# Optimization experiments

Measured on AMD Instinct MI355X. Metric: run time of the kernel, lower is better.

The kernel has to match this reference:

```python
import jax, jax.numpy as jnp
import numpy as np

TOP_K = 2

def setup_inputs() -> dict:
    key = jax.random.key(0)
    kx, kg, k1, k2 = jax.random.split(key, 4)
    B, T, D, E, H = 4, 1024, 1024, 8, 2048
    x = jax.random.normal(kx, (B, T, D), dtype=jnp.float32)
    Wg = jax.random.normal(kg, (D, E), dtype=jnp.float32) * 0.02
    W1 = jax.random.normal(k1, (E, D, H), dtype=jnp.float32) * 0.02  # c_fc per expert
    W2 = jax.random.normal(k2, (E, H, D), dtype=jnp.float32) * 0.02  # c_proj per expert
    return {"x": x, "Wg": Wg, "W1": W1, "W2": W2}

def reference(x, Wg, W1, W2):
    B, T, D = x.shape
    E = W1.shape[0]
    # Router: softmax over experts, top-k, renormalize top-k weights
    logits = jnp.einsum('btd,de->bte', x, Wg)          # (B,T,E)
    probs = jax.nn.softmax(logits, axis=-1)
    top_w, top_i = jax.lax.top_k(probs, TOP_K)          # (B,T,K)
    top_w = top_w / (jnp.sum(top_w, axis=-1, keepdims=True) + 1e-8)
    # Combine weights per (token, expert): sum_k top_w[k] * one_hot(top_i[k])
    N = B * T
    oh = jax.nn.one_hot(top_i.reshape(N, TOP_K), E, dtype=x.dtype)   # (N,K,E)
    combine = jnp.sum(oh * top_w.reshape(N, TOP_K)[..., None], axis=1)  # (N,E)
    # Expert MLPs: relu(x W1)^2 W2, evaluated densely and combined (same math)
    xt = x.reshape(N, D)
    h = jnp.einsum('td,edh->teh', xt, W1)               # (N,E,H)
    h = jnp.square(jax.nn.relu(h))
    y = jnp.einsum('teh,ehd->ted', h, W2)               # (N,E,D)
    out = jnp.einsum('te,ted->td', combine, y)          # (N,D)
    return out.reshape(B, T, D)
```

## Files before the change

kernel.cpp:

```cpp
#include <hip/hip_runtime.h>
#include <hip/hip_bf16.h>
#include <stdint.h>

#define NTOK 4096
#define DD 1024
#define EE 8
#define HH 2048
#define BM 128
#define BN 128
#define BK 64
#define MAXRB 72
#define RPAD (MAXRB*BM)
#define GG1 (8*9*(HH/BN))
#define GG2 (8*9*(DD/BN))

typedef __attribute__((ext_vector_type(4))) float f32x4;
typedef __attribute__((ext_vector_type(8))) short bf16x8;

__device__ __forceinline__ void gload16(const void* g, void* l) {
  __builtin_amdgcn_global_load_lds((const __attribute__((address_space(1))) unsigned int*)g,
                                   (__attribute__((address_space(3))) unsigned int*)l, 16, 0, 0);
}

__device__ __forceinline__ uint32_t pack_bf2(float lo, float hi) {
  return ((uint32_t)__bfloat16_as_ushort(__float2bfloat16(hi)) << 16)
       |  (uint32_t)__bfloat16_as_ushort(__float2bfloat16(lo));
}

__device__ __forceinline__ void transpose_body(uint32_t (*T)[33],
    const float* __restrict__ in, __hip_bfloat16* __restrict__ out,
    int R, int C, int tb) {
  int tilesC = C >> 6;
  int tilesPerE = (R >> 6) * tilesC;
  int e = tb / tilesPerE;
  int rem = tb % tilesPerE;
  int tr = rem / tilesC, tc = rem % tilesC;
  const float* src = in + (size_t)e * R * C + (size_t)(tr*64) * C + tc*64;
  int tid = threadIdx.x;
  int c4 = (tid & 15) << 2;
  int r2 = tid >> 4;
  #pragma unroll
  for (int i = 0; i < 2; ++i) {
    int r = r2 + (i << 4);
    const float* p0 = src + (size_t)(2*r) * C + c4;
    float4 a = *(const float4*)p0;
    float4 b = *(const float4*)(p0 + C);
    T[c4+0][r] = pack_bf2(a.x, b.x);
    T[c4+1][r] = pack_bf2(a.y, b.y);
    T[c4+2][r] = pack_bf2(a.z, b.z);
    T[c4+3][r] = pack_bf2(a.w, b.w);
  }
  __syncthreads();
  __hip_bfloat16* dst = out + (size_t)e * R * C + (size_t)(tc*64) * R + tr*64;
  int c  = tid >> 2;
  int ch = (tid & 3) * 8;
  uint32_t v[8];
  #pragma unroll
  for (int j = 0; j < 8; ++j) v[j] = T[c][ch + j];
  uint32_t* dp = (uint32_t*)(dst + (size_t)c * R + ch*2);
  #pragma unroll
  for (int j = 0; j < 8; ++j) dp[j] = v[j];
}

__global__ __launch_bounds__(256) void mega_kernel(const float* __restrict__ x,
    const float* __restrict__ Wg,
    int* __restrict__ topE, float* __restrict__ topW, int* __restrict__ counts64,
    const float* __restrict__ W1, __hip_bfloat16* __restrict__ W1bT) {
  __shared__ __align__(16) char smem[8448];
  int b = blockIdx.x;
  if (b < NTOK) {
    int t = b;
    int tid = threadIdx.x;
    const float* xr = x + (size_t)t * DD;
    double acc[EE];
    #pragma unroll
    for (int e = 0; e < EE; ++e) acc[e] = 0.0;
    #pragma unroll
    for (int i = 0; i < DD/256; ++i) {
      int d = tid + i*256;
      float xv = xr[d];
      float4 w0 = *(const float4*)(Wg + (size_t)d*EE);
      float4 w1 = *(const float4*)(Wg + (size_t)d*EE + 4);
      double xd = (double)xv;
      acc[0] += xd * (double)w0.x; acc[1] += xd * (double)w0.y;
      acc[2] += xd * (double)w0.z; acc[3] += xd * (double)w0.w;
      acc[4] += xd * (double)w1.x; acc[5] += xd * (double)w1.y;
      acc[6] += xd * (double)w1.z; acc[7] += xd * (double)w1.w;
    }
    #pragma unroll
    for (int e = 0; e < EE; ++e) {
      double v = acc[e];
      #pragma unroll
      for (int off = 32; off > 0; off >>= 1) v += __shfl_down(v, off, 64);
      acc[e] = v;
    }
    double (*sAcc)[EE] = (double(*)[EE])smem;
    int lane = tid & 63, w = tid >> 6;
    if (lane == 0) {
      #pragma unroll
      for (int e = 0; e < EE; ++e) sAcc[w][e] = acc[e];
    }
    __syncthreads();
    if (tid == 0) {
      double s[EE];
      #pragma unroll
      for (int e = 0; e < EE; ++e)
        s[e] = sAcc[0][e] + sAcc[1][e] + sAcc[2][e] + sAcc[3][e];
      double mx = s[0];
      #pragma unroll
      for (int e = 1; e < EE; ++e) mx = fmax(mx, s[e]);
      double p[EE], Z = 0.0;
      #pragma unroll
      for (int e = 0; e < EE; ++e) { p[e] = exp(s[e] - mx); Z += p[e]; }
      #pragma unroll
      for (int e = 0; e < EE; ++e) p[e] /= Z;
      int i0 = 0;
      #pragma unroll
      for (int e = 1; e < EE; ++e) if (p[e] > p[i0]) i0 = e;
      int i1 = -1;
      #pragma unroll
      for (int e = 0; e < EE; ++e) { if (e == i0) continue; if (i1 < 0 || p[e] > p[i1]) i1 = e; }
      double sm = p[i0] + p[i1] + 1e-8;
      topE[t*2]   = i0; topE[t*2+1] = i1;
      topW[t*2]   = (float)(p[i0] / sm);
      topW[t*2+1] = (float)(p[i1] / sm);
      int slot = (b & 63) * 16;
      atomicAdd(&counts64[slot + i0], 1);
      atomicAdd(&counts64[slot + i1], 1);
    }
  } else {
    transpose_body((uint32_t(*)[33])smem, W1, W1bT, DD, HH, b - NTOK);
  }
}

__global__ __launch_bounds__(1024) void assign_kernel(const int* __restrict__ counts64,
    const int* __restrict__ topE, const float* __restrict__ topW,
    int* __restrict__ po, int* __restrict__ nRB, int* __restrict__ rbExpert,
    int* __restrict__ pairsTok, float* __restrict__ pairsW, int* __restrict__ slotOf) {
  __shared__ int cnt[EE];
  __shared__ int base[EE];
  __shared__ int wcnt[16][EE];
  int tid = threadIdx.x, wv = tid >> 6, lane = tid & 63;
  if (tid < EE) {
    int s = 0;
    #pragma unroll
    for (int k = 0; k < 64; ++k) s += counts64[k*16 + tid];
    cnt[tid] = s;
  }
  for (int i = tid; i < RPAD; i += 1024) pairsTok[i] = -1;
  __syncthreads();
  if (tid == 0) {
    int off = 0;
    for (int e = 0; e < EE; ++e) {
      po[e] = off;
      off += ((cnt[e] + BM - 1) / BM) * BM;
    }
    po[EE] = off;
    *nRB = off / BM;
    int rb = 0;
    for (int e = 0; e < EE; ++e) {
      int nb = (cnt[e] + BM - 1) / BM;
      for (int b = 0; b < nb; ++b) rbExpert[rb++] = e;
    }
  }
  __syncthreads();
  if (tid < EE) base[tid] = po[tid];
  __syncthreads();
  for (int it = 0; it < 2*NTOK/1024; ++it) {
    int p = it*1024 + tid;
    int e = topE[p];
    int myrank = 0;
    #pragma unroll
    for (int ee = 0; ee < EE; ++ee) {
      unsigned long long b = __ballot(e == ee);
      if (ee == e) myrank = __popcll(b & ((1ull << lane) - 1ull));
      if (lane == 0) wcnt[wv][ee] = __popcll(b);
    }
    __syncthreads();
    int wbase = 0;
    for (int w2 = 0; w2 < wv; ++w2) wbase += wcnt[w2][e];
    int slot = base[e] + wbase + myrank;
    pairsTok[slot] = p >> 1;
    pairsW[slot]   = topW[p];
    slotOf[p]      = slot;
    __syncthreads();
    if (tid < EE) {
      int s2 = 0;
      #pragma unroll
      for (int w2 = 0; w2 < 16; ++w2) s2 += wcnt[w2][tid];
      base[tid] += s2;
    }
    __syncthreads();
  }
}

__global__ __launch_bounds__(256) void gather_kernel(const float* __restrict__ x,
    const int* __restrict__ slotOf, __hip_bfloat16* __restrict__ Xg) {
  int t = blockIdx.x;
  int s0 = slotOf[2*t], s1 = slotOf[2*t+1];
  const float* xr = x + (size_t)t * DD;
  int i = threadIdx.x;
  float4 v = ((const float4*)xr)[i];
  ushort4 b;
  b.x = __bfloat16_as_ushort(__float2bfloat16(v.x));
  b.y = __bfloat16_as_ushort(__float2bfloat16(v.y));
  b.z = __bfloat16_as_ushort(__float2bfloat16(v.z));
  b.w = __bfloat16_as_ushort(__float2bfloat16(v.w));
  ((ushort4*)(Xg + (size_t)s0 * DD))[i] = b;
  ((ushort4*)(Xg + (size_t)s1 * DD))[i] = b;
}

template<int EPI, int KDIM, int NTOT>
__device__ __forceinline__ void gemm_body(char* smem, int bid,
    const __hip_bfloat16* __restrict__ A, const __hip_bfloat16* __restrict__ Ball,
    __hip_bfloat16* __restrict__ Cbf, float* __restrict__ Cf,
    const int* __restrict__ nRB, const int* __restrict__ rbExpert,
    const int* __restrict__ pairsTok, const float* __restrict__ pairsW) {
  int nrb = *nRB;
  int cpx = (nrb + 7) >> 3;
  int xcd = bid & 7;
  int slot = bid >> 3;
  int lr = slot % 9;
  int nb = slot / 9;
  int rb = xcd * cpx + lr;
  if (lr >= cpx || rb >= nrb) return;
  int e = rbExpert[rb];
  const __hip_bfloat16* Ag = A + (size_t)rb * BM * KDIM;
  const __hip_bfloat16* Bg = Ball + (size_t)e * NTOT * KDIM + (size_t)nb * BN * KDIM;
  __hip_bfloat16* As = (__hip_bfloat16*)smem;
  __hip_bfloat16* Bs = (__hip_bfloat16*)(smem + 16384);
  int*   sTok = (int*)(smem + 32768);
  float* sW   = (float*)(smem + 32768 + 512);
  int tid = threadIdx.x;
  if (EPI == 1 && tid < BM) {
    sTok[tid] = pairsTok[rb*BM + tid];
    sW[tid]   = pairsW[rb*BM + tid];
  }
  int lane = tid & 63;
  int wid = tid >> 6;
  int wr = wid >> 1, wc = wid & 1;
  int l15 = lane & 15;
  int lhi = lane >> 4;
  f32x4 acc[4][4] = {};
  int srow  = tid >> 3;
  int scol8 = (tid & 7) * 8;
  for (int kt = 0; kt < KDIM / BK; ++kt) {
    #pragma unroll
    for (int i = 0; i < 4; ++i) {
      int r = srow + 32*i;
      int sc = scol8 ^ ((r & 7) << 3);
      gload16(Ag + (size_t)r * KDIM + kt*BK + sc, (char*)As + i*4096 + tid*16);
      gload16(Bg + (size_t)r * KDIM + kt*BK + sc, (char*)Bs + i*4096 + tid*16);
    }
    __syncthreads();
    #pragma unroll
    for (int kk = 0; kk < 2; ++kk) {
      bf16x8 af[4], bfr[4];
      int kb = kk*64 + lhi*16;
      #pragma unroll
      for (int m = 0; m < 4; ++m) {
        int row = wr*64 + m*16 + l15;
        af[m] = *(const bf16x8*)((const char*)As + row*128 + (kb ^ ((row & 7) << 4)));
      }
      #pragma unroll
      for (int n = 0; n < 4; ++n) {
        int row = wc*64 + n*16 + l15;
        bfr[n] = *(const bf16x8*)((const char*)Bs + row*128 + (kb ^ ((row & 7) << 4)));
      }
      #pragma unroll
      for (int m = 0; m < 4; ++m)
        #pragma unroll
        for (int n = 0; n < 4; ++n)
          acc[m][n] = __builtin_amdgcn_mfma_f32_16x16x32_bf16(af[m], bfr[n], acc[m][n], 0, 0, 0);
    }
    __syncthreads();
  }
  if (EPI == 0) {
    #pragma unroll
    for (int m = 0; m < 4; ++m) {
      int row = rb*BM + wr*64 + m*16 + lhi*4;
      #pragma unroll
      for (int n = 0; n < 4; ++n) {
        int col = nb*BN + wc*64 + n*16 + l15;
        #pragma unroll
        for (int j = 0; j < 4; ++j) {
          float v = fmaxf(acc[m][n][j], 0.0f);
          Cbf[(size_t)(row + j) * NTOT + col] = __float2bfloat16(v * v);
        }
      }
    }
  } else {
    #pragma unroll
    for (int m = 0; m < 4; ++m) {
      int rloc = wr*64 + m*16 + lhi*4;
      #pragma unroll
      for (int j = 0; j < 4; ++j) {
        int tok = sTok[rloc + j];
        if (tok < 0) continue;
        float w = sW[rloc + j];
        #pragma unroll
        for (int n = 0; n < 4; ++n) {
          int col = nb*BN + wc*64 + n*16 + l15;
          atomicAdd(Cf + (size_t)tok * NTOT + col, w * acc[m][n][j]);
        }
      }
    }
  }
}

__global__ __launch_bounds__(256, 4)
void gemm1_fused(const __hip_bfloat16* __restrict__ Xg,
                 const __hip_bfloat16* __restrict__ W1bT,
                 __hip_bfloat16* __restrict__ Hbuf,
                 const int* __restrict__ nRB, const int* __restrict__ rbExpert,
                 const int* __restrict__ pairsTok, const float* __restrict__ pairsW,
                 const float* __restrict__ W2, __hip_bfloat16* __restrict__ W2bT) {
  __shared__ __align__(16) char smem[33*1024 + 1024];
  int bid = blockIdx.x;
  if (bid < GG1) {
    gemm_body<0, DD, HH>(smem, bid, Xg, W1bT, Hbuf, nullptr,
                         nRB, rbExpert, pairsTok, pairsW);
  } else {
    transpose_body((uint32_t(*)[33])smem, W2, W2bT, HH, DD, bid - GG1);
  }
}

__global__ __launch_bounds__(256, 4)
void gemm2_kernel(const __hip_bfloat16* __restrict__ Hbuf,
                  const __hip_bfloat16* __restrict__ W2bT,
                  float* __restrict__ out,
                  const int* __restrict__ nRB, const int* __restrict__ rbExpert,
                  const int* __restrict__ pairsTok, const float* __restrict__ pairsW) {
  __shared__ __align__(16) char smem[33*1024 + 1024];
  gemm_body<1, HH, DD>(smem, blockIdx.x, Hbuf, W2bT, nullptr, out,
                       nRB, rbExpert, pairsTok, pairsW);
}


extern "C" void kernel_launch(void* const* d_in, const int* in_sizes, int n_in,
                              void* d_out, int out_size, void* d_ws, size_t ws_size,
                              hipStream_t stream) {
  const float* x  = (const float*)d_in[0];
  const float* Wg = (const float*)d_in[1];
  const float* W1 = (const float*)d_in[2];
  const float* W2 = (const float*)d_in[3];
  float* out = (float*)d_out;
  char* ws = (char*)d_ws;

  int*   po       = (int*)(ws + 128);
  int*   nRB      = (int*)(ws + 192);
  int*   rbExpert = (int*)(ws + 256);
  int*   counts64 = (int*)(ws + 4096);
  float* topW     = (float*)(ws + 40960);
  int*   pairsTok = (int*)(ws + 73728);
  float* pairsW   = (float*)(ws + 110592);
  int*   slotOf   = (int*)(ws + 147456);
  int*   topE     = (int*)(ws + 180224);
  __hip_bfloat16* Xg   = (__hip_bfloat16*)(ws + 262144);
  __hip_bfloat16* Hbuf = (__hip_bfloat16*)(ws + 19136512);
  __hip_bfloat16* W1bT = (__hip_bfloat16*)(ws + 56885248);
  __hip_bfloat16* W2bT = (__hip_bfloat16*)(ws + 90439680);

  hipMemsetAsync(d_out, 0, (size_t)out_size * sizeof(float), stream);
  hipMemsetAsync(ws, 0, 8192, stream);

  mega_kernel<<<NTOK + 4096, 256, 0, stream>>>(x, Wg, topE, topW, counts64, W1, W1bT);
  assign_kernel<<<1, 1024, 0, stream>>>(counts64, topE, topW, po, nRB, rbExpert,
                                        pairsTok, pairsW, slotOf);
  gather_kernel<<<NTOK, 256, 0, stream>>>(x, slotOf, Xg);

  gemm1_fused<<<GG1 + 4096, 256, 0, stream>>>(Xg, W1bT, Hbuf, nRB, rbExpert,
                                              pairsTok, pairsW, W2, W2bT);
  gemm2_kernel<<<GG2, 256, 0, stream>>>(Hbuf, W2bT, out, nRB, rbExpert,
                                        pairsTok, pairsW);
}
```

Before: 192.2 us.

## Double-buffer LDS tiles with BK=32 and overlap global loads with MFMA

Replaces the single-buffered BK=64 main loop with a double-buffered BK=32 loop. The next tile's global-to-LDS loads are issued before computing the current tile, with an explicit vmcnt wait and raw s_barrier calls. The swizzle is adjusted for the 64-byte row pitch. This is meant to hide global load latency behind MFMA work, at the cost of twice as many barriers per K and smaller MFMA bursts per stage.

```diff
diff --git a/kernel.cpp b/kernel.cpp
--- a/kernel.cpp
+++ b/kernel.cpp
@@ -8,7 +8,6 @@
 #define HH 2048
 #define BM 128
 #define BN 128
-#define BK 64
 #define MAXRB 72
 #define RPAD (MAXRB*BM)
 #define GG1 (8*9*(HH/BN))
@@ -227,8 +226,6 @@
   int e = rbExpert[rb];
   const __hip_bfloat16* Ag = A + (size_t)rb * BM * KDIM;
   const __hip_bfloat16* Bg = Ball + (size_t)e * NTOT * KDIM + (size_t)nb * BN * KDIM;
-  __hip_bfloat16* As = (__hip_bfloat16*)smem;
-  __hip_bfloat16* Bs = (__hip_bfloat16*)(smem + 16384);
   int*   sTok = (int*)(smem + 32768);
   float* sW   = (float*)(smem + 32768 + 512);
   int tid = threadIdx.x;
@@ -242,39 +239,58 @@
   int l15 = lane & 15;
   int lhi = lane >> 4;
   f32x4 acc[4][4] = {};
-  int srow  = tid >> 3;
-  int scol8 = (tid & 7) * 8;
-  for (int kt = 0; kt < KDIM / BK; ++kt) {
-    #pragma unroll
-    for (int i = 0; i < 4; ++i) {
-      int r = srow + 32*i;
-      int sc = scol8 ^ ((r & 7) << 3);
-      gload16(Ag + (size_t)r * KDIM + kt*BK + sc, (char*)As + i*4096 + tid*16);
-      gload16(Bg + (size_t)r * KDIM + kt*BK + sc, (char*)Bs + i*4096 + tid*16);
-    }
-    __syncthreads();
-    #pragma unroll
-    for (int kk = 0; kk < 2; ++kk) {
-      bf16x8 af[4], bfr[4];
-      int kb = kk*64 + lhi*16;
-      #pragma unroll
-      for (int m = 0; m < 4; ++m) {
-        int row = wr*64 + m*16 + l15;
-        af[m] = *(const bf16x8*)((const char*)As + row*128 + (kb ^ ((row & 7) << 4)));
-      }
-      #pragma unroll
-      for (int n = 0; n < 4; ++n) {
-        int row = wc*64 + n*16 + l15;
-        bfr[n] = *(const bf16x8*)((const char*)Bs + row*128 + (kb ^ ((row & 7) << 4)));
-      }
-      #pragma unroll
-      for (int m = 0; m < 4; ++m)
-        #pragma unroll
-        for (int n = 0; n < 4; ++n)
-          acc[m][n] = __builtin_amdgcn_mfma_f32_16x16x32_bf16(af[m], bfr[n], acc[m][n], 0, 0, 0);
-    }
-    __syncthreads();
-  }
+  int srow4  = tid >> 2;
+  int scol16 = tid & 3;
+
+  #define STAGE(buf, kt) {                                                        \
+    _Pragma("unroll")                                                             \
+    for (int i = 0; i < 2; ++i) {                                                 \
+      int row = srow4 + 64*i;                                                     \
+      int sc = 8 * (scol16 ^ ((row >> 1) & 3));    \
+      gload16(Ag + (size_t)row * KDIM + (kt)*32 + sc,                             \
+              smem + (buf)*16384 + i*4096 + tid*16);                              \
+      gload16(Bg + (size_t)row * KDIM + (kt)*32 + sc,                             \
+              smem + (buf)*16384 + 8192 + i*4096 + tid*16);                       \
+    } }
+
+  #define COMPUTE(buf) {                                                          \
+    bf16x8 af[4], bfr[4];                                                         \
+    _Pragma("unroll")                                                             \
+    for (int m = 0; m < 4; ++m) {                                                 \
+      int row = wr*64 + m*16 + l15;                                               \
+      af[m] = *(const bf16x8*)(smem + (buf)*16384 + row*64 +                      \
+                               ((lhi*16) ^ (((row >> 1) & 3) << 4)));             \
+    }                                                                             \
+    _Pragma("unroll")                                                             \
+    for (int n = 0; n < 4; ++n) {                                                 \
+      int row = wc*64 + n*16 + l15;                                               \
+      bfr[n] = *(const bf16x8*)(smem + (buf)*16384 + 8192 + row*64 +              \
+                                ((lhi*16) ^ (((row >> 1) & 3) << 4)));            \
+    }                                                                             \
+    _Pragma("unroll")                                                             \
+    for (int m = 0; m < 4; ++m)                                                   \
+      _Pragma("unroll")                                                           \
+      for (int n = 0; n < 4; ++n)                                                 \
+        acc[m][n] = __builtin_amdgcn_mfma_f32_16x16x32_bf16(af[m], bfr[n],        \
+                                                            acc[m][n], 0, 0, 0); \
+    }
+
+  constexpr int NT = KDIM / 32;
+  STAGE(0, 0);
+  for (int kt = 0; kt < NT; ++kt) {
+    if (kt + 1 < NT) {
+      STAGE((kt + 1) & 1, kt + 1);
+      asm volatile("s_waitcnt vmcnt(4)" ::: "memory");
+    } else {
+      asm volatile("s_waitcnt vmcnt(0)" ::: "memory");
+    }
+    __builtin_amdgcn_s_barrier();
+    COMPUTE(kt & 1);
+    __builtin_amdgcn_s_barrier();
+  }
+  #undef STAGE
+  #undef COMPUTE
+
   if (EPI == 0) {
     #pragma unroll
     for (int m = 0; m < 4; ++m) {
```

Result: slower. 198.8 us (+3.5%).

## Fuse bf16 conversion into router and gather token rows inside GEMM1 loads

Applied to the files above, without the earlier changes.

Removes the separate gather kernel. The router kernel now writes a bf16 copy of x, and GEMM1 reads A rows indirectly through the per-slot token index (padding rows map to token 0). This drops one kernel launch and the scattered copy into Xg. In exchange, the A-tile loads in GEMM1 become row-indirect gathers, and the router kernel does scalar 2-byte stores.

```diff
diff --git a/kernel.cpp b/kernel.cpp
--- a/kernel.cpp
+++ b/kernel.cpp
@@ -65,6 +65,7 @@
 __global__ __launch_bounds__(256) void mega_kernel(const float* __restrict__ x,
     const float* __restrict__ Wg,
     int* __restrict__ topE, float* __restrict__ topW, int* __restrict__ counts64,
+    __hip_bfloat16* __restrict__ xbf,
     const float* __restrict__ W1, __hip_bfloat16* __restrict__ W1bT) {
   __shared__ __align__(16) char smem[8448];
   int b = blockIdx.x;
@@ -72,6 +73,7 @@
     int t = b;
     int tid = threadIdx.x;
     const float* xr = x + (size_t)t * DD;
+    __hip_bfloat16* xbr = xbf + (size_t)t * DD;
     double acc[EE];
     #pragma unroll
     for (int e = 0; e < EE; ++e) acc[e] = 0.0;
@@ -79,6 +81,7 @@
     for (int i = 0; i < DD/256; ++i) {
       int d = tid + i*256;
       float xv = xr[d];
+      xbr[d] = __float2bfloat16(xv);
       float4 w0 = *(const float4*)(Wg + (size_t)d*EE);
       float4 w1 = *(const float4*)(Wg + (size_t)d*EE + 4);
       double xd = (double)xv;
@@ -136,7 +139,7 @@
 __global__ __launch_bounds__(1024) void assign_kernel(const int* __restrict__ counts64,
     const int* __restrict__ topE, const float* __restrict__ topW,
     int* __restrict__ po, int* __restrict__ nRB, int* __restrict__ rbExpert,
-    int* __restrict__ pairsTok, float* __restrict__ pairsW, int* __restrict__ slotOf) {
+    int* __restrict__ pairsTok, float* __restrict__ pairsW) {
   __shared__ int cnt[EE];
   __shared__ int base[EE];
   __shared__ int wcnt[16][EE];
@@ -182,7 +185,6 @@
     int slot = base[e] + wbase + myrank;
     pairsTok[slot] = p >> 1;
     pairsW[slot]   = topW[p];
-    slotOf[p]      = slot;
     __syncthreads();
     if (tid < EE) {
       int s2 = 0;
@@ -192,22 +194,6 @@
     }
     __syncthreads();
   }
-}
-
-__global__ __launch_bounds__(256) void gather_kernel(const float* __restrict__ x,
-    const int* __restrict__ slotOf, __hip_bfloat16* __restrict__ Xg) {
-  int t = blockIdx.x;
-  int s0 = slotOf[2*t], s1 = slotOf[2*t+1];
-  const float* xr = x + (size_t)t * DD;
-  int i = threadIdx.x;
-  float4 v = ((const float4*)xr)[i];
-  ushort4 b;
-  b.x = __bfloat16_as_ushort(__float2bfloat16(v.x));
-  b.y = __bfloat16_as_ushort(__float2bfloat16(v.y));
-  b.z = __bfloat16_as_ushort(__float2bfloat16(v.z));
-  b.w = __bfloat16_as_ushort(__float2bfloat16(v.w));
-  ((ushort4*)(Xg + (size_t)s0 * DD))[i] = b;
-  ((ushort4*)(Xg + (size_t)s1 * DD))[i] = b;
 }
 
 template<int EPI, int KDIM, int NTOT>
@@ -225,7 +211,6 @@
   int rb = xcd * cpx + lr;
   if (lr >= cpx || rb >= nrb) return;
   int e = rbExpert[rb];
-  const __hip_bfloat16* Ag = A + (size_t)rb * BM * KDIM;
   const __hip_bfloat16* Bg = Ball + (size_t)e * NTOT * KDIM + (size_t)nb * BN * KDIM;
   __hip_bfloat16* As = (__hip_bfloat16*)smem;
   __hip_bfloat16* Bs = (__hip_bfloat16*)(smem + 16384);
@@ -244,12 +229,23 @@
   f32x4 acc[4][4] = {};
   int srow  = tid >> 3;
   int scol8 = (tid & 7) * 8;
+  const __hip_bfloat16* aRow[4];
+  #pragma unroll
+  for (int i = 0; i < 4; ++i) {
+    int r = srow + 32*i;
+    if (EPI == 0) {
+      int tok = pairsTok[rb*BM + r];
+      aRow[i] = A + (size_t)(tok < 0 ? 0 : tok) * KDIM;
+    } else {
+      aRow[i] = A + (size_t)(rb*BM + r) * KDIM;
+    }
+  }
   for (int kt = 0; kt < KDIM / BK; ++kt) {
     #pragma unroll
     for (int i = 0; i < 4; ++i) {
       int r = srow + 32*i;
       int sc = scol8 ^ ((r & 7) << 3);
-      gload16(Ag + (size_t)r * KDIM + kt*BK + sc, (char*)As + i*4096 + tid*16);
+      gload16(aRow[i] + kt*BK + sc, (char*)As + i*4096 + tid*16);
       gload16(Bg + (size_t)r * KDIM + kt*BK + sc, (char*)Bs + i*4096 + tid*16);
     }
     __syncthreads();
@@ -309,7 +305,7 @@
 }
 
 __global__ __launch_bounds__(256, 4)
-void gemm1_fused(const __hip_bfloat16* __restrict__ Xg,
+void gemm1_fused(const __hip_bfloat16* __restrict__ xbf,
                  const __hip_bfloat16* __restrict__ W1bT,
                  __hip_bfloat16* __restrict__ Hbuf,
                  const int* __restrict__ nRB, const int* __restrict__ rbExpert,
@@ -318,7 +314,7 @@
   __shared__ __align__(16) char smem[33*1024 + 1024];
   int bid = blockIdx.x;
   if (bid < GG1) {
-    gemm_body<0, DD, HH>(smem, bid, Xg, W1bT, Hbuf, nullptr,
+    gemm_body<0, DD, HH>(smem, bid, xbf, W1bT, Hbuf, nullptr,
                          nRB, rbExpert, pairsTok, pairsW);
   } else {
     transpose_body((uint32_t(*)[33])smem, W2, W2bT, HH, DD, bid - GG1);
@@ -354,9 +350,8 @@
   float* topW     = (float*)(ws + 40960);
   int*   pairsTok = (int*)(ws + 73728);
   float* pairsW   = (float*)(ws + 110592);
-  int*   slotOf   = (int*)(ws + 147456);
   int*   topE     = (int*)(ws + 180224);
-  __hip_bfloat16* Xg   = (__hip_bfloat16*)(ws + 262144);
+  __hip_bfloat16* xbf  = (__hip_bfloat16*)(ws + 262144);
   __hip_bfloat16* Hbuf = (__hip_bfloat16*)(ws + 19136512);
   __hip_bfloat16* W1bT = (__hip_bfloat16*)(ws + 56885248);
   __hip_bfloat16* W2bT = (__hip_bfloat16*)(ws + 90439680);
@@ -364,12 +359,12 @@
   hipMemsetAsync(d_out, 0, (size_t)out_size * sizeof(float), stream);
   hipMemsetAsync(ws, 0, 8192, stream);
 
-  mega_kernel<<<NTOK + 4096, 256, 0, stream>>>(x, Wg, topE, topW, counts64, W1, W1bT);
+  mega_kernel<<<NTOK + 4096, 256, 0, stream>>>(x, Wg, topE, topW, counts64,
+                                               xbf, W1, W1bT);
   assign_kernel<<<1, 1024, 0, stream>>>(counts64, topE, topW, po, nRB, rbExpert,
-                                        pairsTok, pairsW, slotOf);
-  gather_kernel<<<NTOK, 256, 0, stream>>>(x, slotOf, Xg);
-
-  gemm1_fused<<<GG1 + 4096, 256, 0, stream>>>(Xg, W1bT, Hbuf, nRB, rbExpert,
+                                        pairsTok, pairsW);
+
+  gemm1_fused<<<GG1 + 4096, 256, 0, stream>>>(xbf, W1bT, Hbuf, nRB, rbExpert,
                                               pairsTok, pairsW, W2, W2bT);
   gemm2_kernel<<<GG2, 256, 0, stream>>>(Hbuf, W2bT, out, nRB, rbExpert,
                                         pairsTok, pairsW);
```

Result: faster. 187.0 us (median of 3 runs) (-2.7%).
